# Kernel tuning notes

Hardware: AMD Instinct MI355X
Metric: run time of the kernel (lower is better)

The kernel has to match this reference:

```python
import jax, jax.numpy as jnp
import numpy as np

B, N, M = 256, 512, 512


def setup_inputs() -> dict:
    key = jax.random.key(0)
    kx, kw, kt = jax.random.split(key, 3)
    x = jax.random.uniform(kx, (B, N), dtype=jnp.float32)
    w = jax.random.uniform(kw, (N, M), dtype=jnp.float32)
    t = jax.random.uniform(kt, (B, M), dtype=jnp.float32)
    return {"x": x, "w": w, "t": t}


def reference(x, w, t):
    # x: [B, N], w: [N, M], t: [B, M]
    x3 = x[:, :, None]   # [B, N, 1]
    t3 = t[:, None, :]   # [B, 1, M]
    w3 = w[None, :, :]   # [1, N, M]

    # relevance of x per (n, m): sum over batch of min(x, t) / sum over batch of x
    rel_x = jnp.minimum(x3, t3).sum(axis=0, keepdims=True) / x3.sum(axis=0, keepdims=True)  # [1, N, M]
    # relevance of w per (b, m): sum over N of min(w, t) / sum over N of w
    rel_w = jnp.minimum(w3, t3).sum(axis=-2, keepdims=True) / w3.sum(axis=-2, keepdims=True)  # [B, 1, M]

    # argmax over the N (inner) dimension
    ind_w = jnp.argmax(jnp.minimum(x3, rel_x), axis=-2)  # [B, M]
    ind_x = jnp.argmax(jnp.minimum(rel_w, w3), axis=-2)  # [B, M]

    # inner_x and inner_w are numerically identical in forward (detach only affects grads)
    inner = jnp.minimum(x3, w3)  # [B, N, M]
    chosen_x = jnp.take_along_axis(inner, ind_x[:, None, :], axis=-2)[:, 0, :]  # [B, M]
    chosen_w = jnp.take_along_axis(inner, ind_w[:, None, :], axis=-2)[:, 0, :]  # [B, M]
    return (chosen_x, chosen_w)
```

## Files before the change

kernel.cpp:

```cpp
#include <hip/hip_runtime.h>

#define B 256
#define N 512
#define M 512
#define BM (B * M)
#define NM (N * M)

__device__ __forceinline__ void tile_tr(const float* __restrict__ src,
                                        float* __restrict__ dst,
                                        int R, int C, int r0, int c0, int tid) {
    __shared__ float s[64][65];
    const int tx = tid & 63, ty = tid >> 6;
    #pragma unroll
    for (int j = 0; j < 8; ++j) {
        int rl = ty * 8 + j;
        s[rl][tx] = src[(r0 + rl) * C + c0 + tx];
    }
    __syncthreads();
    #pragma unroll
    for (int j = 0; j < 8; ++j) {
        int cl = ty * 8 + j;
        dst[(c0 + cl) * R + r0 + tx] = s[tx][cl];
    }
}

__global__ __launch_bounds__(512) void k_pre(const float* __restrict__ x,
                                             const float* __restrict__ w,
                                             const float* __restrict__ t,
                                             float* __restrict__ xT,
                                             float* __restrict__ wT,
                                             float* __restrict__ tT,
                                             float* __restrict__ sum_x,
                                             float* __restrict__ sum_w) {
    const int blk = blockIdx.x, tid = threadIdx.x;
    if (blk < 32) {
        tile_tr(x, xT, B, N, (blk >> 3) * 64, (blk & 7) * 64, tid);
    } else if (blk < 96) {
        int id = blk - 32;
        tile_tr(w, wT, N, M, (id >> 3) * 64, (id & 7) * 64, tid);
    } else if (blk < 128) {
        int id = blk - 96;
        tile_tr(t, tT, B, M, (id >> 3) * 64, (id & 7) * 64, tid);
    } else if (blk == 128) {
        int i = tid;
        double a0 = 0, a1 = 0, a2 = 0, a3 = 0;
        for (int b = 0; b < B; b += 4) {
            a0 += (double)x[(b + 0) * N + i];
            a1 += (double)x[(b + 1) * N + i];
            a2 += (double)x[(b + 2) * N + i];
            a3 += (double)x[(b + 3) * N + i];
        }
        sum_x[i] = (float)((a0 + a1) + (a2 + a3));
    } else {
        int mm = tid;
        double a0 = 0, a1 = 0, a2 = 0, a3 = 0;
        for (int n = 0; n < N; n += 4) {
            a0 += (double)w[(n + 0) * M + mm];
            a1 += (double)w[(n + 1) * M + mm];
            a2 += (double)w[(n + 2) * M + mm];
            a3 += (double)w[(n + 3) * M + mm];
        }
        sum_w[mm] = (float)((a0 + a1) + (a2 + a3));
    }
}

__global__ __launch_bounds__(256) void k_relxA(const float* __restrict__ xT,
                                               const float* __restrict__ t,
                                               float* __restrict__ px) {
    const int tx = threadIdx.x, ty = threadIdx.y;
    const int m0 = blockIdx.x * 32, n0 = blockIdx.y * 32;
    const int bbase = blockIdx.z * 64;
    __shared__ float s_t[32][32];
    __shared__ float s_xn[32][36];
    const int tid = ty * 16 + tx;
    const int sr = tid / 8, sc4 = (tid & 7) * 4;
    const int nA = ty * 2, nB = nA + 1;
    float a00 = 0.f, a01 = 0.f, a10 = 0.f, a11 = 0.f;
    for (int scnk = 0; scnk < 2; ++scnk) {
        const int bb = bbase + scnk * 32;
        __syncthreads();
        *(float4*)&s_t[sr][sc4]  = *(const float4*)&t[(bb + sr) * M + m0 + sc4];
        *(float4*)&s_xn[sr][sc4] = *(const float4*)&xT[(n0 + sr) * B + bb + sc4];
        __syncthreads();
        #pragma unroll 8
        for (int i = 0; i < 32; ++i) {
            float2 tv = *(const float2*)&s_t[i][tx * 2];
            float x0 = s_xn[nA][i];
            float x1 = s_xn[nB][i];
            a00 += fminf(x0, tv.x); a01 += fminf(x0, tv.y);
            a10 += fminf(x1, tv.x); a11 += fminf(x1, tv.y);
        }
    }
    const int base = blockIdx.z * NM;
    const int mA = m0 + tx * 2;
    *(float2*)&px[base + mA * N + n0 + nA]       = make_float2(a00, a10);
    *(float2*)&px[base + (mA + 1) * N + n0 + nA] = make_float2(a01, a11);
}

__global__ __launch_bounds__(512) void k_col(
        const float* __restrict__ x, const float* __restrict__ xT,
        const float* __restrict__ wT, const float* __restrict__ tT,
        const float* __restrict__ px, const float* __restrict__ sum_x,
        const float* __restrict__ sum_w, float* __restrict__ out) {
    const int m = blockIdx.x, tid = threadIdx.x;

    __shared__ float  worig[512];
    __shared__ float  pm[512];
    __shared__ float  wsrt[512];
    __shared__ int    cnt[256];
    __shared__ int    cbase[256];
    __shared__ double bsumI[256];
    __shared__ float  redA[256];
    __shared__ float  redB[256];
    __shared__ float  srx_r[512];
    __shared__ int    srx_n[512];
    __shared__ float  srx_u[512];
    __shared__ int    rcnt[256];
    __shared__ int    rbase[256];
    __shared__ int    rbmax[256];

    const float wv = wT[m * N + tid];
    float rv;
    {
        float p = px[m * N + tid];
        p += px[NM + m * N + tid];
        p += px[2 * NM + m * N + tid];
        p += px[3 * NM + m * N + tid];
        rv = p / sum_x[tid];
    }
    worig[tid] = wv;
    pm[tid] = wv;
    srx_r[tid] = rv;
    if (tid < 256) { cnt[tid] = 0; rcnt[tid] = 0; rbmax[tid] = 0; }
    __syncthreads();

    for (int off = 1; off < 512; off <<= 1) {
        float cur = pm[tid];
        float oth = (tid >= off) ? pm[tid - off] : -1.0f;
        __syncthreads();
        pm[tid] = fmaxf(cur, oth);
        __syncthreads();
    }

    if (tid < 256) {
        redA[tid] = fminf(worig[tid], worig[tid + 256]);
        redB[tid] = fminf(srx_r[tid], srx_r[tid + 256]);
    }
    __syncthreads();
    for (int s2 = 128; s2 > 0; s2 >>= 1) {
        if (tid < s2) {
            redA[tid] = fminf(redA[tid], redA[tid + s2]);
            redB[tid] = fminf(redB[tid], redB[tid + s2]);
        }
        __syncthreads();
    }
    const float wmin = redA[0];
    const float rmin = redB[0];
    __syncthreads();
    if (tid < 256) redB[tid] = fmaxf(srx_r[tid], srx_r[tid + 256]);
    __syncthreads();
    for (int s2 = 128; s2 > 0; s2 >>= 1) {
        if (tid < s2) redB[tid] = fmaxf(redB[tid], redB[tid + s2]);
        __syncthreads();
    }
    const float rmax = redB[0];
    const float wmax = pm[511];

    const float wscale = 255.0f / fmaxf(wmax - wmin, 1e-30f);
    int wk = (int)((wv - wmin) * wscale);
    wk = wk < 0 ? 0 : (wk > 255 ? 255 : wk);
    atomicAdd(&cnt[wk], 1);

    const float rscale = 255.0f / fmaxf(rmax - rmin, 1e-30f);
    int rk;
    { int kv = (int)((rv - rmin) * rscale); kv = kv < 0 ? 0 : (kv > 255 ? 255 : kv); rk = 255 - kv; }
    atomicAdd(&rcnt[rk], 1);
    atomicMax(&rbmax[rk], __float_as_int(rv));
    __syncthreads();

    if (tid < 256) { cbase[tid] = cnt[tid]; rbase[tid] = rcnt[tid]; }
    __syncthreads();
    for (int off = 1; off < 256; off <<= 1) {
        int c1 = 0, c2 = 0, o1 = 0, o2 = 0;
        if (tid < 256) {
            c1 = cbase[tid]; c2 = rbase[tid];
            if (tid >= off) { o1 = cbase[tid - off]; o2 = rbase[tid - off]; }
        }
        __syncthreads();
        if (tid < 256) { cbase[tid] = c1 + o1; rbase[tid] = c2 + o2; }
        __syncthreads();
    }
    if (tid < 256) {
        cbase[tid] -= cnt[tid];
        rbase[tid] -= rcnt[tid];
        cnt[tid] = 0; rcnt[tid] = 0;
    }
    __syncthreads();

    {
        int p1 = cbase[wk] + atomicAdd(&cnt[wk], 1);
        wsrt[p1] = wv;
        int p2 = rbase[rk] + atomicAdd(&rcnt[rk], 1);
        srx_r[p2] = rv;
        srx_n[p2] = tid;
        srx_u[p2] = __int_as_float(rbmax[rk]);
    }
    __syncthreads();

    if (tid < 256) {
        double s = 0.0;
        int st = cbase[tid], e = st + cnt[tid];
        for (int i = st; i < e; ++i) s += (double)wsrt[i];
        bsumI[tid] = s;
    }
    __syncthreads();
    for (int off = 1; off < 256; off <<= 1) {
        double cur = 0.0, oth = 0.0;
        if (tid < 256) { cur = bsumI[tid]; if (tid >= off) oth = bsumI[tid - off]; }
        __syncthreads();
        if (tid < 256) bsumI[tid] = cur + oth;
        __syncthreads();
    }

    if (tid < 256) {
        const int b = tid;
        float bv = -1.0f; int bi = 0;
        for (int i = 0; i < 512; ++i) {
            float u = srx_u[i];
            if (__ballot(u >= bv) == 0ULL) break;
            float r = srx_r[i];
            int   n = srx_n[i];
            float xv = xT[n * B + b];
            float v = fminf(xv, r);
            if (v > bv || (v == bv && n < bi)) { bv = v; bi = n; }
        }
        out[BM + b * M + m] = fminf(x[b * N + bi], worig[bi]);
    } else {
        const int b = tid - 256;
        const float tbm = tT[m * B + b];
        float btf = (tbm - wmin) * wscale;
        int kk; double S;
        if (btf < 0.0f) { kk = 0; S = 0.0; }
        else {
            int bt = (int)btf; bt = bt > 255 ? 255 : bt;
            kk = cbase[bt];
            S = (bt > 0) ? bsumI[bt - 1] : 0.0;
            int e = cbase[bt] + cnt[bt];
            for (int i = cbase[bt]; i < e; ++i) {
                float v = wsrt[i];
                if (v < tbm) { ++kk; S += (double)v; }
            }
        }
        double rw = S + (double)tbm * (double)(512 - kk);
        float c = (float)rw / sum_w[m];
        float tgt = fminf(c, pm[511]);
        int lo = 0, hi = 511;
        while (lo < hi) { int mid = (lo + hi) >> 1; if (pm[mid] >= tgt) hi = mid; else lo = mid + 1; }
        const int ind = lo;
        out[b * M + m] = fminf(x[b * N + ind], worig[ind]);
    }
}

extern "C" void kernel_launch(void* const* d_in, const int* in_sizes, int n_in,
                              void* d_out, int out_size, void* d_ws, size_t ws_size,
                              hipStream_t stream) {
    const float* x = (const float*)d_in[0];
    const float* w = (const float*)d_in[1];
    const float* t = (const float*)d_in[2];
    float* out = (float*)d_out;

    float* ws = (float*)d_ws;
    float* xT    = ws;
    float* wT    = ws + 131072;
    float* tT    = ws + 393216;
    float* sum_x = ws + 524288;
    float* sum_w = ws + 524800;
    float* px    = ws + 525312;

    k_pre  <<<130, 512, 0, stream>>>(x, w, t, xT, wT, tT, sum_x, sum_w);
    k_relxA<<<dim3(16, 16, 4), dim3(16, 16), 0, stream>>>(xT, t, px);
    k_col  <<<512, 512, 0, stream>>>(x, xT, wT, tT, px, sum_x, sum_w, out);
}
```

Before: 100.4 us.

## Merge preprocessing and rel_x partial kernels; use wavefront shuffles for scans

The transpose and sum preprocessing is merged with the rel_x partial-sum computation into one launch of 256-thread blocks. The partial sums now read x directly instead of xT, so the dependency on the transpose disappears. Each thread computes a wider 2x4 tile and stages its results through shared memory for coalesced stores. In the column kernel, the barrier-heavy shared-memory prefix scans and reductions become wavefront shuffle scans with cross-warp fixups, cutting many __syncthreads.

```diff
diff --git a/kernel.cpp b/kernel.cpp
--- a/kernel.cpp
+++ b/kernel.cpp
@@ -6,95 +6,106 @@
 #define BM (B * M)
 #define NM (N * M)
 
-__device__ __forceinline__ void tile_tr(const float* __restrict__ src,
-                                        float* __restrict__ dst,
-                                        int R, int C, int r0, int c0, int tid) {
+__device__ __forceinline__ void tile_tr256(const float* __restrict__ src,
+                                           float* __restrict__ dst,
+                                           int R, int C, int r0, int c0, int tid) {
     __shared__ float s[64][65];
-    const int tx = tid & 63, ty = tid >> 6;
-    #pragma unroll
-    for (int j = 0; j < 8; ++j) {
-        int rl = ty * 8 + j;
+    const int tx = tid & 63, q = tid >> 6;
+    #pragma unroll
+    for (int j = 0; j < 16; ++j) {
+        int rl = q * 16 + j;
         s[rl][tx] = src[(r0 + rl) * C + c0 + tx];
     }
     __syncthreads();
     #pragma unroll
-    for (int j = 0; j < 8; ++j) {
-        int cl = ty * 8 + j;
+    for (int j = 0; j < 16; ++j) {
+        int cl = q * 16 + j;
         dst[(c0 + cl) * R + r0 + tx] = s[tx][cl];
     }
 }
 
-__global__ __launch_bounds__(512) void k_pre(const float* __restrict__ x,
-                                             const float* __restrict__ w,
-                                             const float* __restrict__ t,
-                                             float* __restrict__ xT,
-                                             float* __restrict__ wT,
-                                             float* __restrict__ tT,
-                                             float* __restrict__ sum_x,
-                                             float* __restrict__ sum_w) {
+__global__ __launch_bounds__(256) void k_a(const float* __restrict__ x,
+                                           const float* __restrict__ w,
+                                           const float* __restrict__ t,
+                                           float* __restrict__ xT,
+                                           float* __restrict__ wT,
+                                           float* __restrict__ tT,
+                                           float* __restrict__ sum_x,
+                                           float* __restrict__ sum_w,
+                                           float* __restrict__ px) {
     const int blk = blockIdx.x, tid = threadIdx.x;
-    if (blk < 32) {
-        tile_tr(x, xT, B, N, (blk >> 3) * 64, (blk & 7) * 64, tid);
-    } else if (blk < 96) {
-        int id = blk - 32;
-        tile_tr(w, wT, N, M, (id >> 3) * 64, (id & 7) * 64, tid);
-    } else if (blk < 128) {
-        int id = blk - 96;
-        tile_tr(t, tT, B, M, (id >> 3) * 64, (id & 7) * 64, tid);
-    } else if (blk == 128) {
-        int i = tid;
-        double a0 = 0, a1 = 0, a2 = 0, a3 = 0;
-        for (int b = 0; b < B; b += 4) {
-            a0 += (double)x[(b + 0) * N + i];
-            a1 += (double)x[(b + 1) * N + i];
-            a2 += (double)x[(b + 2) * N + i];
-            a3 += (double)x[(b + 3) * N + i];
-        }
-        sum_x[i] = (float)((a0 + a1) + (a2 + a3));
+    if (blk < 512) {
+        const int z   = blk >> 7;
+        const int rem = blk & 127;
+        const int m0 = (rem & 7) * 64;
+        const int n0 = (rem >> 3) * 32;
+        const int tx = tid & 15, ty = tid >> 4;
+        __shared__ float s_t[32][64];
+        __shared__ float s_x[32][36];
+        const int sr = tid >> 3, sc = tid & 7;
+        float aA0 = 0.f, aA1 = 0.f, aA2 = 0.f, aA3 = 0.f;
+        float aB0 = 0.f, aB1 = 0.f, aB2 = 0.f, aB3 = 0.f;
+        const int nA = ty * 2, nB = nA + 1;
+        for (int scnk = 0; scnk < 2; ++scnk) {
+            const int bb = z * 64 + scnk * 32;
+            __syncthreads();
+            *(float4*)&s_t[sr][sc * 8]     = *(const float4*)&t[(bb + sr) * M + m0 + sc * 8];
+            *(float4*)&s_t[sr][sc * 8 + 4] = *(const float4*)&t[(bb + sr) * M + m0 + sc * 8 + 4];
+            *(float4*)&s_x[sr][sc * 4]     = *(const float4*)&x[(bb + sr) * N + n0 + sc * 4];
+            __syncthreads();
+            #pragma unroll 8
+            for (int i = 0; i < 32; ++i) {
+                float4 tv = *(const float4*)&s_t[i][tx * 4];
+                float xA = s_x[i][nA], xB = s_x[i][nB];
+                aA0 += fminf(xA, tv.x); aA1 += fminf(xA, tv.y);
+                aA2 += fminf(xA, tv.z); aA3 += fminf(xA, tv.w);
+                aB0 += fminf(xB, tv.x); aB1 += fminf(xB, tv.y);
+                aB2 += fminf(xB, tv.z); aB3 += fminf(xB, tv.w);
+            }
+        }
+        __syncthreads();
+        float* so = &s_t[0][0];
+        so[(tx * 4 + 0) * 32 + nA] = aA0; so[(tx * 4 + 0) * 32 + nB] = aB0;
+        so[(tx * 4 + 1) * 32 + nA] = aA1; so[(tx * 4 + 1) * 32 + nB] = aB1;
+        so[(tx * 4 + 2) * 32 + nA] = aA2; so[(tx * 4 + 2) * 32 + nB] = aB2;
+        so[(tx * 4 + 3) * 32 + nA] = aA3; so[(tx * 4 + 3) * 32 + nB] = aB3;
+        __syncthreads();
+        const int m_l = tid >> 2, n_l = (tid & 3) * 8;
+        float* dst = &px[z * NM + (m0 + m_l) * N + n0 + n_l];
+        *(float4*)&dst[0] = *(const float4*)&so[m_l * 32 + n_l];
+        *(float4*)&dst[4] = *(const float4*)&so[m_l * 32 + n_l + 4];
+    } else if (blk < 544) {
+        int id = blk - 512;
+        tile_tr256(x, xT, B, N, (id >> 3) * 64, (id & 7) * 64, tid);
+    } else if (blk < 608) {
+        int id = blk - 544;
+        tile_tr256(w, wT, N, M, (id >> 3) * 64, (id & 7) * 64, tid);
+    } else if (blk < 640) {
+        int id = blk - 608;
+        tile_tr256(t, tT, B, M, (id >> 3) * 64, (id & 7) * 64, tid);
+    } else if (blk == 640) {
+        for (int i = tid; i < N; i += 256) {
+            double a0 = 0, a1 = 0, a2 = 0, a3 = 0;
+            for (int b = 0; b < B; b += 4) {
+                a0 += (double)x[(b + 0) * N + i];
+                a1 += (double)x[(b + 1) * N + i];
+                a2 += (double)x[(b + 2) * N + i];
+                a3 += (double)x[(b + 3) * N + i];
+            }
+            sum_x[i] = (float)((a0 + a1) + (a2 + a3));
+        }
     } else {
-        int mm = tid;
-        double a0 = 0, a1 = 0, a2 = 0, a3 = 0;
-        for (int n = 0; n < N; n += 4) {
-            a0 += (double)w[(n + 0) * M + mm];
-            a1 += (double)w[(n + 1) * M + mm];
-            a2 += (double)w[(n + 2) * M + mm];
-            a3 += (double)w[(n + 3) * M + mm];
-        }
-        sum_w[mm] = (float)((a0 + a1) + (a2 + a3));
-    }
-}
-
-__global__ __launch_bounds__(256) void k_relxA(const float* __restrict__ xT,
-                                               const float* __restrict__ t,
-                                               float* __restrict__ px) {
-    const int tx = threadIdx.x, ty = threadIdx.y;
-    const int m0 = blockIdx.x * 32, n0 = blockIdx.y * 32;
-    const int bbase = blockIdx.z * 64;
-    __shared__ float s_t[32][32];
-    __shared__ float s_xn[32][36];
-    const int tid = ty * 16 + tx;
-    const int sr = tid / 8, sc4 = (tid & 7) * 4;
-    const int nA = ty * 2, nB = nA + 1;
-    float a00 = 0.f, a01 = 0.f, a10 = 0.f, a11 = 0.f;
-    for (int scnk = 0; scnk < 2; ++scnk) {
-        const int bb = bbase + scnk * 32;
-        __syncthreads();
-        *(float4*)&s_t[sr][sc4]  = *(const float4*)&t[(bb + sr) * M + m0 + sc4];
-        *(float4*)&s_xn[sr][sc4] = *(const float4*)&xT[(n0 + sr) * B + bb + sc4];
-        __syncthreads();
-        #pragma unroll 8
-        for (int i = 0; i < 32; ++i) {
-            float2 tv = *(const float2*)&s_t[i][tx * 2];
-            float x0 = s_xn[nA][i];
-            float x1 = s_xn[nB][i];
-            a00 += fminf(x0, tv.x); a01 += fminf(x0, tv.y);
-            a10 += fminf(x1, tv.x); a11 += fminf(x1, tv.y);
-        }
-    }
-    const int base = blockIdx.z * NM;
-    const int mA = m0 + tx * 2;
-    *(float2*)&px[base + mA * N + n0 + nA]       = make_float2(a00, a10);
-    *(float2*)&px[base + (mA + 1) * N + n0 + nA] = make_float2(a01, a11);
+        for (int mm = tid; mm < M; mm += 256) {
+            double a0 = 0, a1 = 0, a2 = 0, a3 = 0;
+            for (int n = 0; n < N; n += 4) {
+                a0 += (double)w[(n + 0) * M + mm];
+                a1 += (double)w[(n + 1) * M + mm];
+                a2 += (double)w[(n + 2) * M + mm];
+                a3 += (double)w[(n + 3) * M + mm];
+            }
+            sum_w[mm] = (float)((a0 + a1) + (a2 + a3));
+        }
+    }
 }
 
 __global__ __launch_bounds__(512) void k_col(
@@ -103,74 +114,62 @@
         const float* __restrict__ px, const float* __restrict__ sum_x,
         const float* __restrict__ sum_w, float* __restrict__ out) {
     const int m = blockIdx.x, tid = threadIdx.x;
-
-    __shared__ float  worig[512];
-    __shared__ float  pm[512];
-    __shared__ float  wsrt[512];
-    __shared__ int    cnt[256];
-    __shared__ int    cbase[256];
+    const int lane = tid & 63, wid = tid >> 6;
+
+    __shared__ float  worig[512], pm[512], wsrt[512];
+    __shared__ float  srx_r[512], srx_u[512];
+    __shared__ int    srx_n[512];
+    __shared__ int    cnt[256], cbase[256], cslot[256];
+    __shared__ int    rcnt[256], rbase[256], rslot[256], rbmax[256];
     __shared__ double bsumI[256];
-    __shared__ float  redA[256];
-    __shared__ float  redB[256];
-    __shared__ float  srx_r[512];
-    __shared__ int    srx_n[512];
-    __shared__ float  srx_u[512];
-    __shared__ int    rcnt[256];
-    __shared__ int    rbase[256];
-    __shared__ int    rbmax[256];
+    __shared__ float  wtotmax[8], red3[3][8];
+    __shared__ int    ctot[4], rtot[4];
+    __shared__ double btot[4];
 
     const float wv = wT[m * N + tid];
-    float rv;
+    float p = px[m * N + tid];
+    p += px[NM + m * N + tid];
+    p += px[2 * NM + m * N + tid];
+    p += px[3 * NM + m * N + tid];
+    const float rv = p / sum_x[tid];
+    worig[tid] = wv;
+    if (tid < 256) { cnt[tid] = 0; rcnt[tid] = 0; cslot[tid] = 0; rslot[tid] = 0; rbmax[tid] = 0; }
+
+    float pmv = wv;
+    #pragma unroll
+    for (int off = 1; off < 64; off <<= 1) {
+        float o = __shfl_up(pmv, off, 64);
+        if (lane >= off) pmv = fmaxf(pmv, o);
+    }
+    if (lane == 63) wtotmax[wid] = pmv;
+    float wmn = wv, rmn = rv, rmx = rv;
+    #pragma unroll
+    for (int off = 32; off > 0; off >>= 1) {
+        wmn = fminf(wmn, __shfl_xor(wmn, off, 64));
+        rmn = fminf(rmn, __shfl_xor(rmn, off, 64));
+        rmx = fmaxf(rmx, __shfl_xor(rmx, off, 64));
+    }
+    if (lane == 0) { red3[0][wid] = wmn; red3[1][wid] = rmn; red3[2][wid] = rmx; }
+    __syncthreads();
+
     {
-        float p = px[m * N + tid];
-        p += px[NM + m * N + tid];
-        p += px[2 * NM + m * N + tid];
-        p += px[3 * NM + m * N + tid];
-        rv = p / sum_x[tid];
-    }
-    worig[tid] = wv;
-    pm[tid] = wv;
-    srx_r[tid] = rv;
-    if (tid < 256) { cnt[tid] = 0; rcnt[tid] = 0; rbmax[tid] = 0; }
-    __syncthreads();
-
-    for (int off = 1; off < 512; off <<= 1) {
-        float cur = pm[tid];
-        float oth = (tid >= off) ? pm[tid - off] : -1.0f;
-        __syncthreads();
-        pm[tid] = fmaxf(cur, oth);
-        __syncthreads();
-    }
-
-    if (tid < 256) {
-        redA[tid] = fminf(worig[tid], worig[tid + 256]);
-        redB[tid] = fminf(srx_r[tid], srx_r[tid + 256]);
-    }
-    __syncthreads();
-    for (int s2 = 128; s2 > 0; s2 >>= 1) {
-        if (tid < s2) {
-            redA[tid] = fminf(redA[tid], redA[tid + s2]);
-            redB[tid] = fminf(redB[tid], redB[tid + s2]);
-        }
-        __syncthreads();
-    }
-    const float wmin = redA[0];
-    const float rmin = redB[0];
-    __syncthreads();
-    if (tid < 256) redB[tid] = fmaxf(srx_r[tid], srx_r[tid + 256]);
-    __syncthreads();
-    for (int s2 = 128; s2 > 0; s2 >>= 1) {
-        if (tid < s2) redB[tid] = fmaxf(redB[tid], redB[tid + s2]);
-        __syncthreads();
-    }
-    const float rmax = redB[0];
-    const float wmax = pm[511];
+        float om = -1e30f;
+        for (int j = 0; j < wid; ++j) om = fmaxf(om, wtotmax[j]);
+        pm[tid] = fmaxf(pmv, om);
+    }
+    float wmin = red3[0][0], rmin = red3[1][0], rmax = red3[2][0], wmax = wtotmax[0];
+    #pragma unroll
+    for (int j = 1; j < 8; ++j) {
+        wmin = fminf(wmin, red3[0][j]);
+        rmin = fminf(rmin, red3[1][j]);
+        rmax = fmaxf(rmax, red3[2][j]);
+        wmax = fmaxf(wmax, wtotmax[j]);
+    }
 
     const float wscale = 255.0f / fmaxf(wmax - wmin, 1e-30f);
     int wk = (int)((wv - wmin) * wscale);
     wk = wk < 0 ? 0 : (wk > 255 ? 255 : wk);
     atomicAdd(&cnt[wk], 1);
-
     const float rscale = 255.0f / fmaxf(rmax - rmin, 1e-30f);
     int rk;
     { int kv = (int)((rv - rmin) * rscale); kv = kv < 0 ? 0 : (kv > 255 ? 255 : kv); rk = 255 - kv; }
@@ -178,49 +177,50 @@
     atomicMax(&rbmax[rk], __float_as_int(rv));
     __syncthreads();
 
-    if (tid < 256) { cbase[tid] = cnt[tid]; rbase[tid] = rcnt[tid]; }
-    __syncthreads();
-    for (int off = 1; off < 256; off <<= 1) {
-        int c1 = 0, c2 = 0, o1 = 0, o2 = 0;
-        if (tid < 256) {
-            c1 = cbase[tid]; c2 = rbase[tid];
-            if (tid >= off) { o1 = cbase[tid - off]; o2 = rbase[tid - off]; }
-        }
-        __syncthreads();
-        if (tid < 256) { cbase[tid] = c1 + o1; rbase[tid] = c2 + o2; }
-        __syncthreads();
-    }
-    if (tid < 256) {
-        cbase[tid] -= cnt[tid];
-        rbase[tid] -= rcnt[tid];
-        cnt[tid] = 0; rcnt[tid] = 0;
-    }
-    __syncthreads();
-
-    {
-        int p1 = cbase[wk] + atomicAdd(&cnt[wk], 1);
-        wsrt[p1] = wv;
-        int p2 = rbase[rk] + atomicAdd(&rcnt[rk], 1);
-        srx_r[p2] = rv;
-        srx_n[p2] = tid;
-        srx_u[p2] = __int_as_float(rbmax[rk]);
-    }
-    __syncthreads();
-
-    if (tid < 256) {
-        double s = 0.0;
+    int myc = (tid < 256) ? cnt[tid] : rcnt[tid - 256];
+    int incl = myc;
+    #pragma unroll
+    for (int off = 1; off < 64; off <<= 1) {
+        int o = __shfl_up(incl, off, 64);
+        if (lane >= off) incl += o;
+    }
+    if (lane == 63) { if (wid < 4) ctot[wid] = incl; else rtot[wid - 4] = incl; }
+    __syncthreads();
+    if (tid < 256) {
+        int eo = 0;
+        for (int j = 0; j < wid; ++j) eo += ctot[j];
+        cbase[tid] = eo + incl - myc;
+    } else {
+        int eo = 0, w2 = wid - 4;
+        for (int j = 0; j < w2; ++j) eo += rtot[j];
+        rbase[tid - 256] = eo + incl - myc;
+    }
+    __syncthreads();
+
+    { int p1 = cbase[wk] + atomicAdd(&cslot[wk], 1); wsrt[p1] = wv; }
+    { int p2 = rbase[rk] + atomicAdd(&rslot[rk], 1);
+      srx_r[p2] = rv; srx_n[p2] = tid; srx_u[p2] = __int_as_float(rbmax[rk]); }
+    __syncthreads();
+
+    double bincl = 0.0, mysum = 0.0;
+    if (tid < 256) {
         int st = cbase[tid], e = st + cnt[tid];
-        for (int i = st; i < e; ++i) s += (double)wsrt[i];
-        bsumI[tid] = s;
-    }
-    __syncthreads();
-    for (int off = 1; off < 256; off <<= 1) {
-        double cur = 0.0, oth = 0.0;
-        if (tid < 256) { cur = bsumI[tid]; if (tid >= off) oth = bsumI[tid - off]; }
-        __syncthreads();
-        if (tid < 256) bsumI[tid] = cur + oth;
-        __syncthreads();
-    }
+        for (int i = st; i < e; ++i) mysum += (double)wsrt[i];
+        bincl = mysum;
+        #pragma unroll
+        for (int off = 1; off < 64; off <<= 1) {
+            double o = __shfl_up(bincl, off, 64);
+            if (lane >= off) bincl += o;
+        }
+        if (lane == 63) btot[wid] = bincl;
+    }
+    __syncthreads();
+    if (tid < 256) {
+        double eo = 0.0;
+        for (int j = 0; j < wid; ++j) eo += btot[j];
+        bsumI[tid] = eo + bincl;
+    }
+    __syncthreads();
 
     if (tid < 256) {
         const int b = tid;
@@ -277,7 +277,6 @@
     float* sum_w = ws + 524800;
     float* px    = ws + 525312;
 
-    k_pre  <<<130, 512, 0, stream>>>(x, w, t, xT, wT, tT, sum_x, sum_w);
-    k_relxA<<<dim3(16, 16, 4), dim3(16, 16), 0, stream>>>(xT, t, px);
-    k_col  <<<512, 512, 0, stream>>>(x, xT, wT, tT, px, sum_x, sum_w, out);
-}
+    k_a  <<<642, 256, 0, stream>>>(x, w, t, xT, wT, tT, sum_x, sum_w, px);
+    k_col<<<512, 512, 0, stream>>>(x, xT, wT, tT, px, sum_x, sum_w, out);
+}
```

After: 105.4 us. 1.05x slower.
